# Kernel optimization log

Measured on AMD Instinct MI355X. Metric: run time of the kernel, lower is better.

## Reference

```python
import jax, jax.numpy as jnp
import numpy as np

B, S, T, D, H_HEADS = 2, 2048, 2048, 1024, 16
HD = D // H_HEADS
EPS = 1e-5


def _ln(x, g, b):
    m = jnp.mean(x, axis=-1, keepdims=True)
    v = jnp.mean(jnp.square(x - m), axis=-1, keepdims=True)
    return g * (x - m) * jax.lax.rsqrt(v + EPS) + b


def _mha(xq, xkv, Wq, bq, Wk, bk, Wv, bv, Wo, bo, causal):
    Bq, Lq, _ = xq.shape
    Lk = xkv.shape[1]
    q = (xq @ Wq + bq).reshape(Bq, Lq, H_HEADS, HD)
    k = (xkv @ Wk + bk).reshape(Bq, Lk, H_HEADS, HD)
    v = (xkv @ Wv + bv).reshape(Bq, Lk, H_HEADS, HD)
    scores = jnp.einsum('bqhd,bkhd->bhqk', q, k) / jnp.sqrt(jnp.asarray(HD, q.dtype))
    if causal:
        mask = jnp.tril(jnp.ones((Lq, Lk), dtype=bool))
        scores = jnp.where(mask, scores, jnp.asarray(-1e9, scores.dtype))
    p = jax.nn.softmax(scores, axis=-1)
    o = jnp.einsum('bhqk,bkhd->bqhd', p, v).reshape(Bq, Lq, D)
    return o @ Wo + bo


def setup_inputs() -> dict:
    key = jax.random.key(0)
    ks = jax.random.split(key, 24)
    s = 0.02
    def w(i):
        return jax.random.normal(ks[i], (D, D), jnp.float32) * s
    inp = {
        'S0': jax.random.normal(ks[20], (B, S, D), jnp.float32),
        'H': jax.random.normal(ks[21], (B, T, D), jnp.float32),
        'Wq1': w(0), 'bq1': jnp.zeros((D,)), 'Wk1': w(1), 'bk1': jnp.zeros((D,)),
        'Wv1': w(2), 'bv1': jnp.zeros((D,)), 'Wo1': w(3), 'bo1': jnp.zeros((D,)),
        'ln1_g': jnp.ones((D,)), 'ln1_b': jnp.zeros((D,)),
        'Wq2': w(4), 'bq2': jnp.zeros((D,)), 'Wk2': w(5), 'bk2': jnp.zeros((D,)),
        'Wv2': w(6), 'bv2': jnp.zeros((D,)), 'Wo2': w(7), 'bo2': jnp.zeros((D,)),
        'ln2_g': jnp.ones((D,)), 'ln2_b': jnp.zeros((D,)),
        'Wf': w(8), 'bf': jnp.zeros((D,)),
        'ln3_g': jnp.ones((D,)), 'ln3_b': jnp.zeros((D,)),
    }
    return inp


def reference(S0, H, Wq1, bq1, Wk1, bk1, Wv1, bv1, Wo1, bo1, ln1_g, ln1_b,
              Wq2, bq2, Wk2, bk2, Wv2, bv2, Wo2, bo2, ln2_g, ln2_b,
              Wf, bf, ln3_g, ln3_b):
    # masked (causal) self-attention + add&norm
    a1 = _mha(S0, S0, Wq1, bq1, Wk1, bk1, Wv1, bv1, Wo1, bo1, causal=True)
    S1 = _ln(S0 + a1, ln1_g, ln1_b)
    # cross-attention over encoder output H + add&norm
    a2 = _mha(S1, H, Wq2, bq2, Wk2, bk2, Wv2, bv2, Wo2, bo2, causal=False)
    S2 = _ln(S1 + a2, ln2_g, ln2_b)
    # FFN (single Linear) + add&norm
    S3 = _ln(S2 + (S2 @ Wf + bf), ln3_g, ln3_b)
    return S3
```

## Files before the change

kernel.cpp:

```cpp
#include <hip/hip_runtime.h>
#include <hip/hip_bf16.h>
#include <cstdint>
#include <cstddef>


#define D_DIM 1024
#define SEQ   2048
#define NHEAD 16
#define HDIM  64
#define MROWS 4096

typedef __attribute__((ext_vector_type(8)))  short bf16x8;
typedef __attribute__((ext_vector_type(4)))  float f32x4;
typedef __attribute__((ext_vector_type(16))) float f32x16;
typedef __attribute__((ext_vector_type(4)))  unsigned int u32x4;

static __device__ __forceinline__ short f2bf(float x) {
    __hip_bfloat16 h = __float2bfloat16(x);
    return *reinterpret_cast<short*>(&h);
}

static __device__ __forceinline__ unsigned int cvtpk(float lo, float hi2) {
    unsigned int r;
    asm("v_cvt_pk_bf16_f32 %0, %1, %2" : "=v"(r) : "v"(lo), "v"(hi2));
    return r;
}

#define GLOAD_LDS16(g, l)                                                     \
    __builtin_amdgcn_global_load_lds(                                         \
        (const __attribute__((address_space(1))) unsigned int*)(g),           \
        (__attribute__((address_space(3))) unsigned int*)(l), 16, 0, 0)

struct WPtrs { const float* p[9]; };

__global__ __launch_bounds__(256) void prep_kernel(
    WPtrs wp, short* __restrict__ Wt,
    const float* __restrict__ s0, const float* __restrict__ hx,
    short* __restrict__ d0, short* __restrict__ d1,
    const float* __restrict__ bq1, const float* __restrict__ bk1,
    const float* __restrict__ bv1, const float* __restrict__ bk2,
    const float* __restrict__ bv2, float* __restrict__ cb1,
    float* __restrict__ cb2)
{
    __shared__ float tl[64][65];
    const int t = threadIdx.x;
    const int id = blockIdx.x;
    if (id < 2304) {
        const int z = id >> 8, rem = id & 255;
        const float* src = wp.p[z];
        short* dst = Wt + (size_t)z * D_DIM * D_DIM;
        const int r0 = (rem >> 4) * 64;
        const int c0 = (rem & 15) * 64;
        #pragma unroll
        for (int i = 0; i < 4; ++i) {
            int row = i * 16 + (t >> 4);
            int col = (t & 15) * 4;
            float4 v = *(const float4*)(src + (size_t)(r0 + row) * D_DIM + c0 + col);
            tl[row][col + 0] = v.x; tl[row][col + 1] = v.y;
            tl[row][col + 2] = v.z; tl[row][col + 3] = v.w;
        }
        __syncthreads();
        #pragma unroll
        for (int i = 0; i < 4; ++i) {
            int nrow = i * 16 + (t >> 4);
            int kcol = (t & 15) * 4;
            ushort4 o;
            o.x = (unsigned short)f2bf(tl[kcol + 0][nrow]);
            o.y = (unsigned short)f2bf(tl[kcol + 1][nrow]);
            o.z = (unsigned short)f2bf(tl[kcol + 2][nrow]);
            o.w = (unsigned short)f2bf(tl[kcol + 3][nrow]);
            *(ushort4*)(dst + (size_t)(c0 + nrow) * D_DIM + r0 + kcol) = o;
        }
    } else if (id < 6400) {
        const int cid = id - 2304;
        const bool second = cid >= 2048;
        const float* src = second ? hx : s0;
        short* dst = second ? d1 : d0;
        size_t i = ((size_t)(cid - (second ? 2048 : 0)) * 256 + t) * 8;
        float4 a = *(const float4*)(src + i);
        float4 b = *(const float4*)(src + i + 4);
        bf16x8 o;
        o[0] = f2bf(a.x); o[1] = f2bf(a.y); o[2] = f2bf(a.z); o[3] = f2bf(a.w);
        o[4] = f2bf(b.x); o[5] = f2bf(b.y); o[6] = f2bf(b.z); o[7] = f2bf(b.w);
        *(bf16x8*)(dst + i) = o;
    } else {
        const int i = (id - 6400) * 256 + t;
        if      (i < 1024) cb1[i] = bq1[i];
        else if (i < 2048) cb1[i] = bk1[i - 1024];
        else if (i < 3072) cb1[i] = bv1[i - 2048];
        else if (i < 4096) cb2[i - 3072] = bk2[i - 3072];
        else               cb2[i - 3072] = bv2[i - 4096];
    }
}

__device__ __forceinline__ void gemm_qkv_body(
    short* __restrict__ As_, short* __restrict__ Bs_,
    const short* __restrict__ A, const short* __restrict__ Bt,
    const float* __restrict__ bias,
    short* __restrict__ Qh, short* __restrict__ Kh, short* __restrict__ Vh,
    int col0, float qscale, int bx, int by)
{
    const int t = threadIdx.x;
    const int wave = t >> 6, lane = t & 63;
    const int wm = wave >> 1, wn = wave & 1;
    const int m0 = bx * 128, n0 = by * 128;
    const int l15 = lane & 15, l4 = lane >> 4;
    const int lrow = lane >> 2, lcol = (lane & 3) * 8;
    f32x4 acc[4][4] = {};
    for (int k0 = 0; k0 < D_DIM; k0 += 32) {
        __syncthreads();
        #pragma unroll
        for (int c = 0; c < 2; ++c) {
            int chunk = wave + c * 4;
            int row = chunk * 16 + lrow;
            GLOAD_LDS16(A  + (size_t)(m0 + row) * D_DIM + k0 + lcol,
                        As_ + chunk * 512 + lane * 8);
            GLOAD_LDS16(Bt + (size_t)(n0 + row) * D_DIM + k0 + lcol,
                        Bs_ + chunk * 512 + lane * 8);
        }
        __syncthreads();
        bf16x8 af[4], bfr[4];
        const int kq = l4 * 8;
        #pragma unroll
        for (int i = 0; i < 4; ++i)
            af[i] = *(const bf16x8*)&As_[(wm * 64 + i * 16 + l15) * 32 + kq];
        #pragma unroll
        for (int j = 0; j < 4; ++j)
            bfr[j] = *(const bf16x8*)&Bs_[(wn * 64 + j * 16 + l15) * 32 + kq];
        #pragma unroll
        for (int i = 0; i < 4; ++i)
            #pragma unroll
            for (int j = 0; j < 4; ++j)
                acc[i][j] = __builtin_amdgcn_mfma_f32_16x16x32_bf16(
                    af[i], bfr[j], acc[i][j], 0, 0, 0);
    }
    const int rbase = m0 + wm * 64;
    const int cbase = n0 + wn * 64;
    float bv[4];
    #pragma unroll
    for (int j = 0; j < 4; ++j) bv[j] = bias[cbase + j * 16 + l15];
    #pragma unroll
    for (int i = 0; i < 4; ++i) {
        #pragma unroll
        for (int r = 0; r < 4; ++r) {
            const int grow = rbase + i * 16 + l4 * 4 + r;
            const int b = grow >> 11, s = grow & 2047;
            #pragma unroll
            for (int j = 0; j < 4; ++j) {
                const int vcol = col0 + cbase + j * 16 + l15;
                float v = acc[i][j][r] + bv[j];
                if (vcol < 1024) v *= qscale;
                short* dst = (vcol < 1024) ? Qh : ((vcol < 2048) ? Kh : Vh);
                const int h = (vcol >> 6) & 15, hd = vcol & 63;
                dst[((size_t)(b * 16 + h) * SEQ + s) * HDIM + hd] = f2bf(v);
            }
        }
    }
}

__global__ __launch_bounds__(256) void gemm_qkv_kernel(
    const short* __restrict__ A, const short* __restrict__ Bt,
    const float* __restrict__ bias,
    short* __restrict__ Qh, short* __restrict__ Kh, short* __restrict__ Vh,
    int col0, float qscale)
{
    __shared__ short lds[8192];
    gemm_qkv_body(lds, lds + 4096, A, Bt, bias, Qh, Kh, Vh,
                  col0, qscale, blockIdx.x, blockIdx.y);
}

__global__ __launch_bounds__(256) void gemm_resid_kernel(
    const short* __restrict__ A, const short* __restrict__ Bt,
    const float* __restrict__ bias, const float* __restrict__ resid,
    float* __restrict__ Cout)
{
    __shared__ short As[128 * 32];
    __shared__ short Bs[64 * 32];
    const int t = threadIdx.x;
    const int wave = t >> 6, lane = t & 63;
    const int wm = wave >> 1, wn = wave & 1;
    const int m0 = blockIdx.x * 128, n0 = blockIdx.y * 64;
    const int l15 = lane & 15, l4 = lane >> 4;
    const int lrow = lane >> 2, lcol = (lane & 3) * 8;
    f32x4 acc[4][2] = {};
    for (int k0 = 0; k0 < D_DIM; k0 += 32) {
        __syncthreads();
        #pragma unroll
        for (int c = 0; c < 2; ++c) {
            int chunk = wave + c * 4;
            int row = chunk * 16 + lrow;
            GLOAD_LDS16(A + (size_t)(m0 + row) * D_DIM + k0 + lcol,
                        As + chunk * 512 + lane * 8);
        }
        {
            int row = wave * 16 + lrow;
            GLOAD_LDS16(Bt + (size_t)(n0 + row) * D_DIM + k0 + lcol,
                        Bs + wave * 512 + lane * 8);
        }
        __syncthreads();
        bf16x8 af[4], bfr[2];
        const int kq = l4 * 8;
        #pragma unroll
        for (int i = 0; i < 4; ++i)
            af[i] = *(const bf16x8*)&As[(wm * 64 + i * 16 + l15) * 32 + kq];
        #pragma unroll
        for (int j = 0; j < 2; ++j)
            bfr[j] = *(const bf16x8*)&Bs[(wn * 32 + j * 16 + l15) * 32 + kq];
        #pragma unroll
        for (int i = 0; i < 4; ++i)
            #pragma unroll
            for (int j = 0; j < 2; ++j)
                acc[i][j] = __builtin_amdgcn_mfma_f32_16x16x32_bf16(
                    af[i], bfr[j], acc[i][j], 0, 0, 0);
    }
    const int rbase = m0 + wm * 64;
    const int cbase = n0 + wn * 32;
    float bv[2];
    #pragma unroll
    for (int j = 0; j < 2; ++j) bv[j] = bias[cbase + j * 16 + l15];
    #pragma unroll
    for (int i = 0; i < 4; ++i) {
        #pragma unroll
        for (int r = 0; r < 4; ++r) {
            const int grow = rbase + i * 16 + l4 * 4 + r;
            #pragma unroll
            for (int j = 0; j < 2; ++j) {
                const int gcol = cbase + j * 16 + l15;
                float v = acc[i][j][r] + bv[j]
                        + resid[(size_t)grow * D_DIM + gcol];
                Cout[(size_t)grow * D_DIM + gcol] = v;
            }
        }
    }
}

template<bool CAUSAL>
__device__ __forceinline__ void attn_body(
    char* ldsb,
    const short* __restrict__ Qh, const short* __restrict__ Kh,
    const short* __restrict__ Vh, short* __restrict__ O, const int id)
{
    const int t = threadIdx.x, wave = t >> 6, lane = t & 63;
    const int q_own = lane & 31, hi = lane >> 5;
    const int bh = ((id & 7) << 2) | ((id >> 3) & 3);
    const int qsel = id >> 5;
    const int b = bh >> 4, h = bh & 15;
    const short* Qp = Qh + (size_t)bh * SEQ * HDIM;
    const short* Kp = Kh + (size_t)bh * SEQ * HDIM;
    const short* Vp = Vh + (size_t)bh * SEQ * HDIM;
    short* Op = O + (size_t)b * SEQ * D_DIM + h * HDIM;

    const int ksrc = (t & 7) ^ ((t >> 3) & 7);
    const int vr2 = (t & 31) * 2, vg = (t >> 5) * 8;
    const int swz = (q_own & 7) << 3;

    bf16x8 ones;
    #pragma unroll
    for (int j = 0; j < 8; ++j) ones[j] = (short)0x3F80;

    const int npm = CAUSAL ? 2 : 1;
    for (int pm = 0; pm < npm; ++pm) {
        const int qt = CAUSAL ? (pm == 0 ? qsel : 15 - qsel) : qsel;
        const int q0 = qt * 128;
        const int qw = q0 + wave * 32;

        bf16x8 qf[4];
        #pragma unroll
        for (int s = 0; s < 4; ++s)
            qf[s] = *(const bf16x8*)(Qp + (size_t)(qw + q_own) * HDIM
                                     + s * 16 + hi * 8);

        int qkb[4], pvb[8], vwb[8], kgb;
        #pragma unroll
        for (int s = 0; s < 4; ++s)
            qkb[s] = q_own * 128 + 2 * ((s * 16 + hi * 8) ^ swz);
        #pragma unroll
        for (int ks = 0; ks < 8; ++ks)
            pvb[ks] = 32768 + q_own * 256 + 2 * ((ks * 16 + hi * 8) ^ swz);
        #pragma unroll
        for (int j = 0; j < 8; ++j)
            vwb[j] = 32768 + (vg + j) * 256 + 2 * (vr2 ^ (j << 3));
        kgb = t * 16;

        f32x16 oacc[2] = {};
        f32x16 lsum = {};
        float m_ = 0.0f;
        const int nkt = CAUSAL ? (qt + 1) : (SEQ / 128);

        bf16x8 va0, vb0, va1, vb1;

        if (pm) __syncthreads();

        #pragma unroll
        for (int c = 0; c < 4; ++c) {
            const int row = c * 32 + (t >> 3);
            GLOAD_LDS16(Kp + (size_t)row * HDIM + ksrc * 8,
                        ldsb + kgb + c * 4096);
        }
        va0 = *(const bf16x8*)(Vp + (size_t)vr2 * HDIM + vg);
        vb0 = *(const bf16x8*)(Vp + (size_t)(vr2 + 1) * HDIM + vg);
        va1 = *(const bf16x8*)(Vp + (size_t)(64 + vr2) * HDIM + vg);
        vb1 = *(const bf16x8*)(Vp + (size_t)(65 + vr2) * HDIM + vg);
        #pragma unroll
        for (int j = 0; j < 8; ++j) {
            unsigned int p0 = ((unsigned int)(unsigned short)vb0[j] << 16)
                            | (unsigned short)va0[j];
            unsigned int p1 = ((unsigned int)(unsigned short)vb1[j] << 16)
                            | (unsigned short)va1[j];
            *(unsigned int*)(ldsb + vwb[j])       = p0;
            *(unsigned int*)(ldsb + vwb[j] + 128) = p1;
        }
        __syncthreads();
        kgb ^= 16384;
        #pragma unroll
        for (int j = 0; j < 8; ++j) vwb[j] ^= 16384;

        for (int kt = 0; kt < nkt; ++kt) {
            const int kbase = kt * 128;
            const bool have_next = (kt + 1 < nkt);

            if (have_next) {
                #pragma unroll
                for (int c = 0; c < 4; ++c) {
                    const int row = kbase + 128 + c * 32 + (t >> 3);
                    GLOAD_LDS16(Kp + (size_t)row * HDIM + ksrc * 8,
                                ldsb + kgb + c * 4096);
                }
                va0 = *(const bf16x8*)(Vp + (size_t)(kbase + 128 + vr2) * HDIM + vg);
                vb0 = *(const bf16x8*)(Vp + (size_t)(kbase + 129 + vr2) * HDIM + vg);
                va1 = *(const bf16x8*)(Vp + (size_t)(kbase + 192 + vr2) * HDIM + vg);
                vb1 = *(const bf16x8*)(Vp + (size_t)(kbase + 193 + vr2) * HDIM + vg);
            }

            f32x16 minit;
            #pragma unroll
            for (int rr = 0; rr < 16; ++rr) minit[rr] = -m_;
            f32x16 sc[4];
            sc[0] = minit; sc[1] = minit; sc[2] = minit; sc[3] = minit;
            __builtin_amdgcn_s_setprio(1);
            #pragma unroll
            for (int kt2 = 0; kt2 < 4; ++kt2) {
                #pragma unroll
                for (int s = 0; s < 4; ++s) {
                    bf16x8 kf = *(const bf16x8*)(ldsb + qkb[s] + kt2 * 4096);
                    sc[kt2] = __builtin_amdgcn_mfma_f32_32x32x16_bf16(
                        kf, qf[s], sc[kt2], 0, 0, 0);
                }
            }
            __builtin_amdgcn_s_setprio(0);

            if (CAUSAL && (kbase + 127 > qw)) {
                #pragma unroll
                for (int kt2 = 0; kt2 < 4; ++kt2)
                    #pragma unroll
                    for (int rr = 0; rr < 16; ++rr) {
                        const int k = kbase + kt2 * 32
                                    + (rr & 3) + 8 * (rr >> 2) + 4 * hi;
                        if (k > qw + q_own) sc[kt2][rr] = -1e30f;
                    }
            }

            float km[4];
            #pragma unroll
            for (int kt2 = 0; kt2 < 4; ++kt2) {
                float t0 = fmaxf(fmaxf(sc[kt2][0],  sc[kt2][1]),  sc[kt2][2]);
                float t1 = fmaxf(fmaxf(sc[kt2][3],  sc[kt2][4]),  sc[kt2][5]);
                float t2 = fmaxf(fmaxf(sc[kt2][6],  sc[kt2][7]),  sc[kt2][8]);
                float t3 = fmaxf(fmaxf(sc[kt2][9],  sc[kt2][10]), sc[kt2][11]);
                float t4 = fmaxf(fmaxf(sc[kt2][12], sc[kt2][13]), sc[kt2][14]);
                float u  = fmaxf(fmaxf(t0, t1), t2);
                float v  = fmaxf(fmaxf(t3, t4), sc[kt2][15]);
                km[kt2] = fmaxf(u, v);
            }
            float smax = fmaxf(fmaxf(fmaxf(km[0], km[1]), km[2]), km[3]);
            smax = fmaxf(smax, __shfl_xor(smax, 32));

            if (!__all(smax <= 8.0f)) {
                const float sp = fmaxf(smax, 0.f);
                const float corr = exp2f(-sp);
                lsum[0] *= corr;
                #pragma unroll
                for (int ht = 0; ht < 2; ++ht)
                    #pragma unroll
                    for (int rr = 0; rr < 16; ++rr)
                        oacc[ht][rr] *= corr;
                #pragma unroll
                for (int kt2 = 0; kt2 < 4; ++kt2)
                    #pragma unroll
                    for (int rr = 0; rr < 16; ++rr)
                        sc[kt2][rr] -= sp;
                m_ += sp;
            }

            #pragma unroll
            for (int kt2 = 0; kt2 < 4; ++kt2)
                #pragma unroll
                for (int rr = 0; rr < 16; ++rr)
                    sc[kt2][rr] = exp2f(sc[kt2][rr]);

            u32x4 paw[8];
            #pragma unroll
            for (int kt2 = 0; kt2 < 4; ++kt2) {
                unsigned int w0a = cvtpk(sc[kt2][0],  sc[kt2][1]);
                unsigned int w0b = cvtpk(sc[kt2][2],  sc[kt2][3]);
                unsigned int w1a = cvtpk(sc[kt2][4],  sc[kt2][5]);
                unsigned int w1b = cvtpk(sc[kt2][6],  sc[kt2][7]);
                unsigned int w2a = cvtpk(sc[kt2][8],  sc[kt2][9]);
                unsigned int w2b = cvtpk(sc[kt2][10], sc[kt2][11]);
                unsigned int w3a = cvtpk(sc[kt2][12], sc[kt2][13]);
                unsigned int w3b = cvtpk(sc[kt2][14], sc[kt2][15]);
                asm("v_permlane32_swap_b32 %0, %1" : "+v"(w0a), "+v"(w1a));
                asm("v_permlane32_swap_b32 %0, %1" : "+v"(w0b), "+v"(w1b));
                asm("v_permlane32_swap_b32 %0, %1" : "+v"(w2a), "+v"(w3a));
                asm("v_permlane32_swap_b32 %0, %1" : "+v"(w2b), "+v"(w3b));
                paw[kt2 * 2 + 0][0] = w0a; paw[kt2 * 2 + 0][1] = w0b;
                paw[kt2 * 2 + 0][2] = w1a; paw[kt2 * 2 + 0][3] = w1b;
                paw[kt2 * 2 + 1][0] = w2a; paw[kt2 * 2 + 1][1] = w2b;
                paw[kt2 * 2 + 1][2] = w3a; paw[kt2 * 2 + 1][3] = w3b;
            }

            __builtin_amdgcn_s_setprio(1);
            #pragma unroll
            for (int ks = 0; ks < 8; ++ks) {
                union { u32x4 u; bf16x8 bv8; } pc;
                pc.u = paw[ks];
                bf16x8 vf0 = *(const bf16x8*)(ldsb + pvb[ks]);
                oacc[0] = __builtin_amdgcn_mfma_f32_32x32x16_bf16(
                    vf0, pc.bv8, oacc[0], 0, 0, 0);
                bf16x8 vf1 = *(const bf16x8*)(ldsb + pvb[ks] + 8192);
                oacc[1] = __builtin_amdgcn_mfma_f32_32x32x16_bf16(
                    vf1, pc.bv8, oacc[1], 0, 0, 0);
                lsum = __builtin_amdgcn_mfma_f32_32x32x16_bf16(
                    ones, pc.bv8, lsum, 0, 0, 0);
            }
            __builtin_amdgcn_s_setprio(0);

            if (have_next) {
                #pragma unroll
                for (int j = 0; j < 8; ++j) {
                    unsigned int p0 = ((unsigned int)(unsigned short)vb0[j] << 16)
                                    | (unsigned short)va0[j];
                    unsigned int p1 = ((unsigned int)(unsigned short)vb1[j] << 16)
                                    | (unsigned short)va1[j];
                    *(unsigned int*)(ldsb + vwb[j])       = p0;
                    *(unsigned int*)(ldsb + vwb[j] + 128) = p1;
                }
                __syncthreads();
            }
            kgb ^= 16384;
            #pragma unroll
            for (int s = 0; s < 4; ++s) qkb[s] ^= 16384;
            #pragma unroll
            for (int ks = 0; ks < 8; ++ks) pvb[ks] ^= 16384;
            #pragma unroll
            for (int j = 0; j < 8; ++j) vwb[j] ^= 16384;
        }

        const float inv = 1.0f / lsum[0];
        const int grow = qw + q_own;
        #pragma unroll
        for (int ht = 0; ht < 2; ++ht)
            #pragma unroll
            for (int j = 0; j < 4; ++j) {
                ushort4 o;
                o.x = (unsigned short)f2bf(oacc[ht][4 * j + 0] * inv);
                o.y = (unsigned short)f2bf(oacc[ht][4 * j + 1] * inv);
                o.z = (unsigned short)f2bf(oacc[ht][4 * j + 2] * inv);
                o.w = (unsigned short)f2bf(oacc[ht][4 * j + 3] * inv);
                *(ushort4*)&Op[(size_t)grow * D_DIM + ht * 32 + 8 * j + 4 * hi] = o;
            }
    }
}

template<bool CAUSAL>
__global__ __launch_bounds__(256, 2) void attn_mfma_kernel(
    const short* __restrict__ Qh, const short* __restrict__ Kh,
    const short* __restrict__ Vh, short* __restrict__ O)
{
    __shared__ short lds[32768];
    attn_body<CAUSAL>((char*)lds, Qh, Kh, Vh, O, blockIdx.x);
}

__global__ __launch_bounds__(256, 2) void fused_cattn_kv2_kernel(
    const short* __restrict__ Qh, const short* __restrict__ Kh,
    const short* __restrict__ Vh, short* __restrict__ O,
    const short* __restrict__ A2, const short* __restrict__ Bt2,
    const float* __restrict__ bias2,
    short* __restrict__ Kh2, short* __restrict__ Vh2)
{
    __shared__ short lds[32768];
    if (blockIdx.x < 256) {
        attn_body<true>((char*)lds, Qh, Kh, Vh, O, blockIdx.x);
    } else {
        const int bx2 = blockIdx.x - 256;
        gemm_qkv_body(lds, lds + 4096, A2, Bt2, bias2,
                      nullptr, Kh2, Vh2, 1024, 1.0f, bx2 & 31, bx2 >> 5);
    }
}

__global__ __launch_bounds__(256) void ln_kernel(
    const float* __restrict__ X, const float* __restrict__ g,
    const float* __restrict__ bb, float* __restrict__ outf,
    short* __restrict__ outb)
{
    const int row = blockIdx.x;
    const int t = threadIdx.x;
    const float* x = X + (size_t)row * D_DIM;
    float4 v = *(const float4*)(x + (t << 2));
    float s  = v.x + v.y + v.z + v.w;
    float sq = v.x * v.x + v.y * v.y + v.z * v.z + v.w * v.w;
    #pragma unroll
    for (int off = 1; off < 64; off <<= 1) {
        s  += __shfl_xor(s, off);
        sq += __shfl_xor(sq, off);
    }
    __shared__ float ss[4], ssq[4];
    const int wid = t >> 6, lane = t & 63;
    if (lane == 0) { ss[wid] = s; ssq[wid] = sq; }
    __syncthreads();
    s  = ss[0] + ss[1] + ss[2] + ss[3];
    sq = ssq[0] + ssq[1] + ssq[2] + ssq[3];
    const float mean = s * (1.0f / 1024.0f);
    const float var  = sq * (1.0f / 1024.0f) - mean * mean;
    const float inv  = rsqrtf(var + 1e-5f);
    float4 gv = *(const float4*)(g  + (t << 2));
    float4 bv = *(const float4*)(bb + (t << 2));
    float4 o;
    o.x = gv.x * (v.x - mean) * inv + bv.x;
    o.y = gv.y * (v.y - mean) * inv + bv.y;
    o.z = gv.z * (v.z - mean) * inv + bv.z;
    o.w = gv.w * (v.w - mean) * inv + bv.w;
    if (outf) *(float4*)(outf + (size_t)row * D_DIM + (t << 2)) = o;
    if (outb) {
        ushort4 ob;
        ob.x = (unsigned short)f2bf(o.x); ob.y = (unsigned short)f2bf(o.y);
        ob.z = (unsigned short)f2bf(o.z); ob.w = (unsigned short)f2bf(o.w);
        *(ushort4*)(outb + (size_t)row * D_DIM + (t << 2)) = ob;
    }
}

extern "C" void kernel_launch(void* const* d_in, const int* in_sizes, int n_in,
                              void* d_out, int out_size, void* d_ws, size_t ws_size,
                              hipStream_t stream)
{
    (void)in_sizes; (void)n_in; (void)out_size; (void)ws_size;
    const float* S0f = (const float*)d_in[0];
    const float* Hf  = (const float*)d_in[1];
    const float* bq1 = (const float*)d_in[3];
    const float* bk1 = (const float*)d_in[5];
    const float* bv1 = (const float*)d_in[7];
    const float* bo1 = (const float*)d_in[9];
    const float* g1  = (const float*)d_in[10]; const float* b1 = (const float*)d_in[11];
    const float* bq2 = (const float*)d_in[13];
    const float* bk2 = (const float*)d_in[15];
    const float* bv2 = (const float*)d_in[17];
    const float* bo2 = (const float*)d_in[19];
    const float* g2  = (const float*)d_in[20]; const float* b2 = (const float*)d_in[21];
    const float* bff = (const float*)d_in[23];
    const float* g3  = (const float*)d_in[24]; const float* b3 = (const float*)d_in[25];

    char* ws = (char*)d_ws;
    size_t off = 0;
    auto alloc = [&](size_t bytes) { char* p = ws + off; off += (bytes + 255) & ~(size_t)255; return p; };
    short* Wt   = (short*)alloc((size_t)9 * D_DIM * D_DIM * 2);
    short* bS0  = (short*)alloc((size_t)MROWS * D_DIM * 2);
    short* bH   = (short*)alloc((size_t)MROWS * D_DIM * 2);
    short* Qhb  = (short*)alloc((size_t)MROWS * D_DIM * 2);
    short* Khb  = (short*)alloc((size_t)MROWS * D_DIM * 2);
    short* Vhb  = (short*)alloc((size_t)MROWS * D_DIM * 2);
    short* Khb2 = (short*)alloc((size_t)MROWS * D_DIM * 2);
    short* Vhb2 = (short*)alloc((size_t)MROWS * D_DIM * 2);
    short* bAO  = (short*)alloc((size_t)MROWS * D_DIM * 2);
    float* X    = (float*)alloc((size_t)MROWS * D_DIM * 4);
    short* bSx  = (short*)alloc((size_t)MROWS * D_DIM * 2);
    float* cb1  = (float*)alloc(3072 * 4);
    float* cb2  = (float*)alloc(2048 * 4);

    const size_t WSTRIDE = (size_t)D_DIM * D_DIM;
    const float QSCALE = 0.125f * 1.44269504088896f;

    WPtrs wp;
    wp.p[0] = (const float*)d_in[2];
    wp.p[1] = (const float*)d_in[4];
    wp.p[2] = (const float*)d_in[6];
    wp.p[3] = (const float*)d_in[8];
    wp.p[4] = (const float*)d_in[12];
    wp.p[5] = (const float*)d_in[14];
    wp.p[6] = (const float*)d_in[16];
    wp.p[7] = (const float*)d_in[18];
    wp.p[8] = (const float*)d_in[22];

    prep_kernel<<<dim3(6420), 256, 0, stream>>>(
        wp, Wt, S0f, Hf, bS0, bH, bq1, bk1, bv1, bk2, bv2, cb1, cb2);

    const dim3 blk(256);
    const dim3 attn_grid_f(512);
    const dim3 resid_grid(32, 16);

    gemm_qkv_kernel<<<dim3(32, 24), blk, 0, stream>>>(
        bS0, Wt, cb1, Qhb, Khb, Vhb, 0, QSCALE);
    fused_cattn_kv2_kernel<<<dim3(768), blk, 0, stream>>>(
        Qhb, Khb, Vhb, bAO, bH, Wt + 5 * WSTRIDE, cb2, Khb2, Vhb2);
    gemm_resid_kernel<<<resid_grid, blk, 0, stream>>>(
        bAO, Wt + 3 * WSTRIDE, bo1, S0f, X);
    ln_kernel<<<MROWS, blk, 0, stream>>>(X, g1, b1, X, bSx);

    gemm_qkv_kernel<<<dim3(32, 8), blk, 0, stream>>>(
        bSx, Wt + 4 * WSTRIDE, bq2, Qhb, Khb, Vhb, 0, QSCALE);
    attn_mfma_kernel<false><<<attn_grid_f, blk, 0, stream>>>(
        Qhb, Khb2, Vhb2, bAO);
    gemm_resid_kernel<<<resid_grid, blk, 0, stream>>>(
        bAO, Wt + 7 * WSTRIDE, bo2, X, X);
    ln_kernel<<<MROWS, blk, 0, stream>>>(X, g2, b2, X, bSx);

    gemm_resid_kernel<<<resid_grid, blk, 0, stream>>>(
        bSx, Wt + 8 * WSTRIDE, bff, X, X);
    ln_kernel<<<MROWS, blk, 0, stream>>>(X, g3, b3, (float*)d_out, nullptr);
}
```

Before: 275.6 us.

## Single-buffer V in fused causal attention kernel to allow three blocks per CU

```diff
diff --git a/kernel.cpp b/kernel.cpp
--- a/kernel.cpp
+++ b/kernel.cpp
@@ -234,7 +234,7 @@
     }
 }
 
-template<bool CAUSAL>
+template<bool CAUSAL, bool VSINGLE>
 __device__ __forceinline__ void attn_body(
     char* ldsb,
     const short* __restrict__ Qh, const short* __restrict__ Kh,
@@ -284,6 +284,7 @@
 
         f32x16 oacc[2] = {};
         f32x16 lsum = {};
+        f32x16 minit = {};
         float m_ = 0.0f;
         const int nkt = CAUSAL ? (qt + 1) : (SEQ / 128);
 
@@ -312,8 +313,10 @@
         }
         __syncthreads();
         kgb ^= 16384;
-        #pragma unroll
-        for (int j = 0; j < 8; ++j) vwb[j] ^= 16384;
+        if (!VSINGLE) {
+            #pragma unroll
+            for (int j = 0; j < 8; ++j) vwb[j] ^= 16384;
+        }
 
         for (int kt = 0; kt < nkt; ++kt) {
             const int kbase = kt * 128;
@@ -332,16 +335,15 @@
                 vb1 = *(const bf16x8*)(Vp + (size_t)(kbase + 193 + vr2) * HDIM + vg);
             }
 
-            f32x16 minit;
-            #pragma unroll
-            for (int rr = 0; rr < 16; ++rr) minit[rr] = -m_;
             f32x16 sc[4];
-            sc[0] = minit; sc[1] = minit; sc[2] = minit; sc[3] = minit;
             __builtin_amdgcn_s_setprio(1);
             #pragma unroll
             for (int kt2 = 0; kt2 < 4; ++kt2) {
-                #pragma unroll
-                for (int s = 0; s < 4; ++s) {
+                bf16x8 kf0 = *(const bf16x8*)(ldsb + qkb[0] + kt2 * 4096);
+                sc[kt2] = __builtin_amdgcn_mfma_f32_32x32x16_bf16(
+                    kf0, qf[0], minit, 0, 0, 0);
+                #pragma unroll
+                for (int s = 1; s < 4; ++s) {
                     bf16x8 kf = *(const bf16x8*)(ldsb + qkb[s] + kt2 * 4096);
                     sc[kt2] = __builtin_amdgcn_mfma_f32_32x32x16_bf16(
                         kf, qf[s], sc[kt2], 0, 0, 0);
@@ -390,6 +392,8 @@
                     for (int rr = 0; rr < 16; ++rr)
                         sc[kt2][rr] -= sp;
                 m_ += sp;
+                #pragma unroll
+                for (int rr = 0; rr < 16; ++rr) minit[rr] = -m_;
             }
 
             #pragma unroll
@@ -436,24 +440,40 @@
             __builtin_amdgcn_s_setprio(0);
 
             if (have_next) {
-                #pragma unroll
-                for (int j = 0; j < 8; ++j) {
-                    unsigned int p0 = ((unsigned int)(unsigned short)vb0[j] << 16)
-                                    | (unsigned short)va0[j];
-                    unsigned int p1 = ((unsigned int)(unsigned short)vb1[j] << 16)
-                                    | (unsigned short)va1[j];
-                    *(unsigned int*)(ldsb + vwb[j])       = p0;
-                    *(unsigned int*)(ldsb + vwb[j] + 128) = p1;
+                if (VSINGLE) {
+                    __syncthreads();
+                    #pragma unroll
+                    for (int j = 0; j < 8; ++j) {
+                        unsigned int p0 = ((unsigned int)(unsigned short)vb0[j] << 16)
+                                        | (unsigned short)va0[j];
+                        unsigned int p1 = ((unsigned int)(unsigned short)vb1[j] << 16)
+                                        | (unsigned short)va1[j];
+                        *(unsigned int*)(ldsb + vwb[j])       = p0;
+                        *(unsigned int*)(ldsb + vwb[j] + 128) = p1;
+                    }
+                    __syncthreads();
+                } else {
+                    #pragma unroll
+                    for (int j = 0; j < 8; ++j) {
+                        unsigned int p0 = ((unsigned int)(unsigned short)vb0[j] << 16)
+                                        | (unsigned short)va0[j];
+                        unsigned int p1 = ((unsigned int)(unsigned short)vb1[j] << 16)
+                                        | (unsigned short)va1[j];
+                        *(unsigned int*)(ldsb + vwb[j])       = p0;
+                        *(unsigned int*)(ldsb + vwb[j] + 128) = p1;
+                    }
+                    __syncthreads();
                 }
-                __syncthreads();
             }
             kgb ^= 16384;
             #pragma unroll
             for (int s = 0; s < 4; ++s) qkb[s] ^= 16384;
-            #pragma unroll
-            for (int ks = 0; ks < 8; ++ks) pvb[ks] ^= 16384;
-            #pragma unroll
-            for (int j = 0; j < 8; ++j) vwb[j] ^= 16384;
+            if (!VSINGLE) {
+                #pragma unroll
+                for (int ks = 0; ks < 8; ++ks) pvb[ks] ^= 16384;
+                #pragma unroll
+                for (int j = 0; j < 8; ++j) vwb[j] ^= 16384;
+            }
         }
 
         const float inv = 1.0f / lsum[0];
@@ -478,19 +498,19 @@
     const short* __restrict__ Vh, short* __restrict__ O)
 {
     __shared__ short lds[32768];
-    attn_body<CAUSAL>((char*)lds, Qh, Kh, Vh, O, blockIdx.x);
-}
-
-__global__ __launch_bounds__(256, 2) void fused_cattn_kv2_kernel(
+    attn_body<CAUSAL, false>((char*)lds, Qh, Kh, Vh, O, blockIdx.x);
+}
+
+__global__ __launch_bounds__(256, 3) void fused_cattn_kv2_kernel(
     const short* __restrict__ Qh, const short* __restrict__ Kh,
     const short* __restrict__ Vh, short* __restrict__ O,
     const short* __restrict__ A2, const short* __restrict__ Bt2,
     const float* __restrict__ bias2,
     short* __restrict__ Kh2, short* __restrict__ Vh2)
 {
-    __shared__ short lds[32768];
+    __shared__ short lds[24576];
     if (blockIdx.x < 256) {
-        attn_body<true>((char*)lds, Qh, Kh, Vh, O, blockIdx.x);
+        attn_body<true, true>((char*)lds, Qh, Kh, Vh, O, blockIdx.x);
     } else {
         const int bx2 = blockIdx.x - 256;
         gemm_qkv_body(lds, lds + 4096, A2, Bt2, bias2,
```

Measured after the change: 338.1 us. 1.23x slower.
